# Optimization experiments

Measured on AMD Instinct MI355X. Metric: run time of the kernel, lower is better.

Reference implementation:

```python
import jax, jax.numpy as jnp
import numpy as np
from jax import lax

B, C, H, W = 4, 256, 64, 64
K = 9          # points
G = 32         # GroupNorm groups
EPS = 1e-5


def base_offset():
    # matches get_base_offset: y = 0, x in [-(K-1)//2 .. K//2], interleaved (y,x)
    bx = jnp.arange(-((K - 1) // 2), K // 2 + 1, dtype=jnp.float32)
    by = jnp.zeros_like(bx)
    return jnp.stack([by, bx], axis=1).reshape(1, 2 * K, 1, 1)


def conv3x3(x, w, b):
    y = lax.conv_general_dilated(x, w, (1, 1), ((1, 1), (1, 1)),
                                 dimension_numbers=('NCHW', 'OIHW', 'NCHW'))
    return y + b[None, :, None, None]


def group_norm(x, gamma, beta):
    b, c, h, w = x.shape
    xg = x.reshape(b, G, c // G, h, w)
    mu = xg.mean(axis=(2, 3, 4), keepdims=True)
    var = xg.var(axis=(2, 3, 4), keepdims=True)
    xn = ((xg - mu) * lax.rsqrt(var + EPS)).reshape(b, c, h, w)
    return xn * gamma[None, :, None, None] + beta[None, :, None, None]


def _deform_sample_one(img, off):
    # img: [C,H,W]; off: [K,2,H,W] (y,x). Kernel [1,K], stride 1, pad (0, K//2).
    c, h, w = img.shape
    base_x = (jnp.arange(K) - K // 2).astype(img.dtype)  # kernel grid x positions
    py = off[:, 0] + jnp.arange(h, dtype=img.dtype)[None, :, None]                 # [K,H,W]
    px = off[:, 1] + jnp.arange(w, dtype=img.dtype)[None, None, :] + base_x[:, None, None]
    y0 = jnp.floor(py)
    x0 = jnp.floor(px)
    wy = py - y0
    wx = px - x0
    flat = img.reshape(c, h * w)

    def corner(yi, xi):
        valid = (yi >= 0) & (yi <= h - 1) & (xi >= 0) & (xi <= w - 1)
        yc = jnp.clip(yi, 0, h - 1).astype(jnp.int32)
        xc = jnp.clip(xi, 0, w - 1).astype(jnp.int32)
        v = flat[:, (yc * w + xc).reshape(-1)].reshape(c, K, h, w)
        return v * valid[None].astype(img.dtype)

    return (corner(y0, x0) * ((1 - wy) * (1 - wx))[None]
            + corner(y0, x0 + 1) * ((1 - wy) * wx)[None]
            + corner(y0 + 1, x0) * (wy * (1 - wx))[None]
            + corner(y0 + 1, x0 + 1) * (wy * wx)[None])  # [C,K,H,W]


def deform_conv(x, offset, w):
    # x [B,C,H,W]; offset [B,2K,H,W]; w [O,C,1,K]; no bias (mmcv DeformConv2d)
    b, _, h, ww = x.shape
    off = offset.reshape(b, K, 2, h, ww)
    cols = jax.vmap(_deform_sample_one)(x, off)  # [B,C,K,H,W]
    return jnp.einsum('bckhw,ock->bohw', cols, w[:, :, 0, :])


def setup_inputs() -> dict:
    key = jax.random.key(0)
    ks = jax.random.split(key, 8)
    return {
        'cls_feat': jax.random.normal(ks[0], (B, C, H, W), jnp.float32),
        'reg_feat': jax.random.normal(ks[1], (B, C, H, W), jnp.float32),
        'offc_w': jax.random.normal(ks[2], (C, C, 3, 3), jnp.float32) * 0.01,
        'offc_b': jnp.zeros((C,), jnp.float32),
        'offc_g': jnp.ones((C,), jnp.float32),
        'offc_bt': jnp.zeros((C,), jnp.float32),
        'offo_w': jax.random.normal(ks[3], (2 * K, C, 3, 3), jnp.float32) * 0.01,
        'offo_b': jnp.zeros((2 * K,), jnp.float32),
        'clsdc_w': jax.random.normal(ks[4], (C, C, 1, K), jnp.float32) / np.sqrt(C * K),
        'cls_g': jnp.ones((C,), jnp.float32),
        'cls_bt': jnp.zeros((C,), jnp.float32),
        'regdc_w': jax.random.normal(ks[5], (C, C, 1, K), jnp.float32) / np.sqrt(C * K),
        'reg_g': jnp.ones((C,), jnp.float32),
        'reg_bt': jnp.zeros((C,), jnp.float32),
    }


def reference(cls_feat, reg_feat, offc_w, offc_b, offc_g, offc_bt,
              offo_w, offo_b, clsdc_w, cls_g, cls_bt, regdc_w, reg_g, reg_bt):
    # offset branch: ConvModule(3x3) -> GN -> ReLU, then 3x3 offset_out head
    t = jax.nn.relu(group_norm(conv3x3(reg_feat, offc_w, offc_b), offc_g, offc_bt))
    pts = conv3x3(t, offo_w, offo_b)          # [B, 2K, H, W]
    off = pts - base_offset()
    cls_out = jax.nn.relu(group_norm(deform_conv(cls_feat, off, clsdc_w), cls_g, cls_bt))
    reg_out = jax.nn.relu(group_norm(deform_conv(reg_feat, off, regdc_w), reg_g, reg_bt))
    return pts, cls_out, reg_out
```

## Files before the change

### kernel.cpp

```cpp
#include <hip/hip_runtime.h>
#include <math.h>

#define BB 4
#define CC 256
#define HH 64
#define WW 64
#define KP 9
#define GG 32
#define HWW (HH*WW)
#define FEL ((size_t)BB*CC*HH*WW)
#define GN_CNT 32768.0f

typedef __bf16 bf16x8 __attribute__((ext_vector_type(8)));
typedef float  f32x4  __attribute__((ext_vector_type(4)));

__device__ __forceinline__ float bflo(unsigned u) {
    union { unsigned u; float f; } x; x.u = u << 16; return x.f;
}
__device__ __forceinline__ float bfhi(unsigned u) {
    union { unsigned u; float f; } x; x.u = u & 0xffff0000u; return x.f;
}

#define VT256_RD(row, P)  (((row) << 8) + ((((P) ^ ((row) & 7))) << 3))
#define VT256_WR(row, u)  (((row) << 8) + (((((u) >> 1) ^ ((row) & 7))) << 3) + (((u) & 1) << 2))
#define VT128_RD(row, P)  (((row) << 7) + ((((P) ^ ((row) & 7))) << 3))
#define VT128_WR(row, u)  (((row) << 7) + (((((u) >> 1) ^ ((row) & 7))) << 3) + (((u) & 1) << 2))

__global__ void prep_all(const float* __restrict__ w1, const float* __restrict__ wc,
                         const float* __restrict__ wr, const float* __restrict__ w18,
                         __bf16* __restrict__ f1, __bf16* __restrict__ fc,
                         __bf16* __restrict__ fr, __bf16* __restrict__ f18,
                         float* __restrict__ stats) {
    int gid = blockIdx.x * 256 + threadIdx.x;
    if (gid < 768) stats[gid] = 0.f;
    const int NW = 589824;
    if (gid < 3 * NW) {
        int which = gid / NW;
        int idx = gid - which * NW;
        int j   = idx & 7;
        int l   = (idx >> 3) & 63;
        int o16 = (idx >> 9) & 15;
        int c0  = (idx >> 13) & 7;
        int k   = idx >> 16;
        int o = o16 * 16 + (l & 15);
        int c = c0 * 32 + (l >> 4) * 8 + j;
        const float* src = (which == 0) ? w1 : ((which == 1) ? wc : wr);
        __bf16* dst = (which == 0) ? f1 : ((which == 1) ? fc : fr);
        dst[idx] = (__bf16)src[(size_t)(o * 256 + c) * 9 + k];
    } else {
        int idx = gid - 3 * NW;
        int j   = idx & 7;
        int l   = (idx >> 3) & 63;
        int o16 = (idx >> 9) & 1;
        int c0  = (idx >> 10) & 7;
        int k   = idx >> 13;
        int o = o16 * 16 + (l & 15);
        int c = c0 * 32 + (l >> 4) * 8 + j;
        float v = (o < 18) ? w18[(size_t)(o * 256 + c) * 9 + k] : 0.f;
        f18[idx] = (__bf16)v;
    }
}

__global__ void transpose_feat(const float* __restrict__ cls,
                               const float* __restrict__ reg,
                               __bf16* __restrict__ out_cls,
                               __bf16* __restrict__ out_reg) {
    __shared__ float tile[64][65];
    int c0 = blockIdx.x * 64;
    int y  = blockIdx.y;
    int b  = blockIdx.z & 3;
    const float* in = (blockIdx.z >> 2) ? reg : cls;
    __bf16* out     = (blockIdx.z >> 2) ? out_reg : out_cls;
    int lx = threadIdx.x & 63;
    int q  = threadIdx.x >> 6;
    for (int j = 0; j < 16; ++j) {
        int ci = q * 16 + j;
        tile[ci][lx] = in[(((size_t)b*CC + c0 + ci)*HH + y)*WW + lx];
    }
    __syncthreads();
    for (int j = 0; j < 16; ++j) {
        int xi = q * 16 + j;
        out[(((size_t)b*HH + y)*WW + xi)*CC + c0 + lx] = (__bf16)tile[lx][xi];
    }
}

__global__ __launch_bounds__(256, 4) void conv1_mfma(
    const __bf16* __restrict__ in_cl,
    const __bf16* __restrict__ wf,
    const float* __restrict__ bias,
    __bf16* __restrict__ t_out,
    float* __restrict__ stats)
{
    __shared__ __bf16 Vt[66 * 256];
    __shared__ float groupStats[64];
    int blk = blockIdx.x;
    int bb = blk & 3;
    int oq = (blk >> 2) & 3;
    int y  = blk >> 4;
    int t  = threadIdx.x;
    int w  = t >> 6;
    int l  = t & 63;
    int quad = l >> 4;
    int l15  = l & 15;
    if (t < 64) groupStats[t] = 0.f;

    const __bf16* inb = in_cl + (size_t)bb * HWW * CC;
    f32x4 acc[4];
    #pragma unroll
    for (int i = 0; i < 4; ++i) acc[i] = (f32x4){0.f, 0.f, 0.f, 0.f};

    for (int ky = 0; ky < 3; ++ky) {
        int yy = y + ky - 1;
        bool yok = (yy >= 0 && yy < HH);
        __syncthreads();
        for (int u = t; u < 66 * 64; u += 256) {
            int xl = u >> 6, cu = u & 63;
            int gx = xl - 1;
            uint2 val = make_uint2(0u, 0u);
            if (yok && gx >= 0 && gx < WW)
                val = *(const uint2*)(inb + ((size_t)(yy * WW + gx)) * CC + cu * 4);
            *(uint2*)&Vt[VT256_WR(xl, cu)] = val;
        }
        __syncthreads();
        #pragma unroll
        for (int kx = 0; kx < 3; ++kx) {
            int k = ky * 3 + kx;
            const bf16x8* wbase = (const bf16x8*)(wf + (size_t)k * 65536);
            for (int c0 = 0; c0 < 8; ++c0) {
                bf16x8 a[4];
                #pragma unroll
                for (int pt = 0; pt < 4; ++pt) {
                    int row = pt * 16 + l15 + kx;
                    a[pt] = *(const bf16x8*)&Vt[VT256_RD(row, c0 * 4 + quad)];
                }
                bf16x8 bfr = wbase[(c0 * 16 + (oq * 4 + w)) * 64 + l];
                #pragma unroll
                for (int pt = 0; pt < 4; ++pt)
                    acc[pt] = __builtin_amdgcn_mfma_f32_16x16x32_bf16(
                        a[pt], bfr, acc[pt], 0, 0, 0);
            }
        }
    }
    {
        int o = oq * 64 + w * 16 + l15;
        float bi = bias[o];
        float s1 = 0.f, s2 = 0.f;
        #pragma unroll
        for (int pt = 0; pt < 4; ++pt)
            #pragma unroll
            for (int r = 0; r < 4; ++r) {
                float v = acc[pt][r] + bi;
                int px = pt * 16 + quad * 4 + r;
                t_out[(((size_t)bb * HH + y) * WW + px) * CC + o] = (__bf16)v;
                s1 += v; s2 += v * v;
            }
        s1 += __shfl_xor(s1, 16, 64); s1 += __shfl_xor(s1, 32, 64);
        s2 += __shfl_xor(s2, 16, 64); s2 += __shfl_xor(s2, 32, 64);
        if (quad == 0) {
            atomicAdd(&groupStats[(o >> 3) * 2],     s1);
            atomicAdd(&groupStats[(o >> 3) * 2 + 1], s2);
        }
    }
    __syncthreads();
    if (t < 64) atomicAdd(&stats[bb * 64 + t], groupStats[t]);
}

__global__ __launch_bounds__(256, 4) void conv18_mfma(
    const __bf16* __restrict__ t_bf,
    const __bf16* __restrict__ wf18,
    const float* __restrict__ bias,
    const float* __restrict__ stats,
    const float* __restrict__ gamma, const float* __restrict__ beta,
    float* __restrict__ pts)
{
    __shared__ __bf16 Vt[34 * 256];
    int blk = blockIdx.x;
    int bb = blk & 3;
    int xh = (blk >> 2) & 1;
    int y  = blk >> 3;
    int t  = threadIdx.x;
    int w  = t >> 6;
    int l  = t & 63;
    int quad = l >> 4;
    int l15  = l & 15;
    int mt   = w & 1;
    int o16  = w >> 1;
    int x0   = xh * 32;
    const __bf16* inb = t_bf + (size_t)bb * HWW * CC;

    int cbase = (t & 63) * 4;
    int g = cbase >> 3;
    float mu = stats[bb * 64 + g * 2]     * (1.f / GN_CNT);
    float ms = stats[bb * 64 + g * 2 + 1] * (1.f / GN_CNT);
    float rs = rsqrtf(ms - mu * mu + 1e-5f);
    float sc[4], sh[4];
    #pragma unroll
    for (int j = 0; j < 4; ++j) {
        float ga = gamma[cbase + j];
        sc[j] = rs * ga;
        sh[j] = beta[cbase + j] - mu * rs * ga;
    }

    f32x4 acc = (f32x4){0.f, 0.f, 0.f, 0.f};

    for (int ky = 0; ky < 3; ++ky) {
        int yy = y + ky - 1;
        bool yok = (yy >= 0 && yy < HH);
        __syncthreads();
        for (int u = t; u < 34 * 64; u += 256) {
            int xl = u >> 6, cu = u & 63;
            int gx = x0 - 1 + xl;
            uint2 val = make_uint2(0u, 0u);
            if (yok && gx >= 0 && gx < WW) {
                uint2 q = *(const uint2*)(inb + ((size_t)(yy * WW + gx)) * CC + cu * 4);
                float v0 = fmaxf(bflo(q.x) * sc[0] + sh[0], 0.f);
                float v1 = fmaxf(bfhi(q.x) * sc[1] + sh[1], 0.f);
                float v2 = fmaxf(bflo(q.y) * sc[2] + sh[2], 0.f);
                float v3 = fmaxf(bfhi(q.y) * sc[3] + sh[3], 0.f);
                __bf16 o4[4] = {(__bf16)v0, (__bf16)v1, (__bf16)v2, (__bf16)v3};
                val = *(const uint2*)o4;
            }
            *(uint2*)&Vt[VT256_WR(xl, cu)] = val;
        }
        __syncthreads();
        #pragma unroll
        for (int kx = 0; kx < 3; ++kx) {
            int k = ky * 3 + kx;
            const bf16x8* wbase = (const bf16x8*)(wf18 + (size_t)k * 8192);
            for (int c0 = 0; c0 < 8; ++c0) {
                int row = mt * 16 + l15 + kx;
                bf16x8 a = *(const bf16x8*)&Vt[VT256_RD(row, c0 * 4 + quad)];
                bf16x8 bfr = wbase[(c0 * 2 + o16) * 64 + l];
                acc = __builtin_amdgcn_mfma_f32_16x16x32_bf16(a, bfr, acc, 0, 0, 0);
            }
        }
    }
    {
        int o = o16 * 16 + l15;
        if (o < 18) {
            float bi = bias[o];
            float4 st;
            st.x = acc[0] + bi;
            st.y = acc[1] + bi;
            st.z = acc[2] + bi;
            st.w = acc[3] + bi;
            *(float4*)(pts + (((size_t)bb*18 + o)*HH + y)*WW + x0 + mt*16 + quad*4) = st;
        }
    }
}

__global__ __launch_bounds__(512, 4) void deform_mfma(
    const __bf16* __restrict__ cls_cl, const __bf16* __restrict__ reg_cl,
    const __bf16* __restrict__ wfc, const __bf16* __restrict__ wfr,
    const float* __restrict__ pts,
    __bf16* __restrict__ out_cls, __bf16* __restrict__ out_reg,
    float* __restrict__ stats)
{
    __shared__ float pairW4[576 * 4];
    __shared__ int   pairO4[576 * 4];
    __shared__ __bf16 Vt[2][64 * 128];
    __shared__ float groupStats[64];

    int blk = blockIdx.x;
    int g8  = blk & 7;
    int which = g8 & 1;
    int bb  = g8 >> 1;
    int y   = blk >> 3;
    const __bf16* featb = (which ? reg_cl : cls_cl) + (size_t)bb * HWW * CC;
    const __bf16* wf    = which ? wfr : wfc;
    __bf16* outp  = which ? out_reg : out_cls;
    float* statsP = stats + 256 + which * 256 + bb * 64;

    int t = threadIdx.x;
    int w = t >> 6;
    int l = t & 63;
    int quad = l >> 4;
    int l15  = l & 15;
    int tp   = t >> 5;
    int cq   = t & 31;

    if (t < 64) groupStats[t] = 0.f;
    for (int j = t; j < 576; j += 512) {
        int k = j >> 6;
        int x = j & 63;
        float py  = pts[(((size_t)bb*18 + 2*k)*HH + y)*WW + x] + (float)y;
        float pxf = pts[(((size_t)bb*18 + 2*k + 1)*HH + y)*WW + x] + (float)x;
        float y0f = floorf(py), x0f = floorf(pxf);
        float wy = py - y0f, wx = pxf - x0f;
        int iy0 = (int)y0f, ix0 = (int)x0f;
        int iy1 = iy0 + 1,  ix1 = ix0 + 1;
        bool vy0 = (iy0 >= 0 && iy0 < HH), vy1 = (iy1 >= 0 && iy1 < HH);
        bool vx0 = (ix0 >= 0 && ix0 < WW), vx1 = (ix1 >= 0 && ix1 < WW);
        int cy0 = min(max(iy0, 0), HH-1), cy1 = min(max(iy1, 0), HH-1);
        int cx0 = min(max(ix0, 0), WW-1), cx1 = min(max(ix1, 0), WW-1);
        pairW4[j*4+0] = (1.f-wy)*(1.f-wx) * ((vy0 && vx0) ? 1.f : 0.f);
        pairW4[j*4+1] = (1.f-wy)*wx       * ((vy0 && vx1) ? 1.f : 0.f);
        pairW4[j*4+2] = wy*(1.f-wx)       * ((vy1 && vx0) ? 1.f : 0.f);
        pairW4[j*4+3] = wy*wx             * ((vy1 && vx1) ? 1.f : 0.f);
        pairO4[j*4+0] = (cy0*WW + cx0)*CC;
        pairO4[j*4+1] = (cy0*WW + cx1)*CC;
        pairO4[j*4+2] = (cy1*WW + cx0)*CC;
        pairO4[j*4+3] = (cy1*WW + cx1)*CC;
    }

    f32x4 acc[2][4];
    #pragma unroll
    for (int i = 0; i < 2; ++i)
        #pragma unroll
        for (int j = 0; j < 4; ++j)
            acc[i][j] = (f32x4){0.f, 0.f, 0.f, 0.f};

    auto stage_loads = [&](int s, uint2 L[4][4], float4 WV[4]) {
        int k = s >> 1, ch = s & 1;
        const __bf16* fb = featb + ch * 128 + cq * 4;
        #pragma unroll
        for (int it = 0; it < 4; ++it) {
            int pxi = it * 16 + tp;
            int j = k * 64 + pxi;
            WV[it] = *(const float4*)&pairW4[j * 4];
            int4 ov = *(const int4*)&pairO4[j * 4];
            L[it][0] = *(const uint2*)(fb + ov.x);
            L[it][1] = *(const uint2*)(fb + ov.y);
            L[it][2] = *(const uint2*)(fb + ov.z);
            L[it][3] = *(const uint2*)(fb + ov.w);
        }
    };
    auto stage_combine = [&](int s, uint2 L[4][4], float4 WV[4]) {
        __bf16* buf = &Vt[s & 1][0];
        #pragma unroll
        for (int it = 0; it < 4; ++it) {
            int pxi = it * 16 + tp;
            float4 wv = WV[it];
            float v0 = wv.x*bflo(L[it][0].x) + wv.y*bflo(L[it][1].x) + wv.z*bflo(L[it][2].x) + wv.w*bflo(L[it][3].x);
            float v1 = wv.x*bfhi(L[it][0].x) + wv.y*bfhi(L[it][1].x) + wv.z*bfhi(L[it][2].x) + wv.w*bfhi(L[it][3].x);
            float v2 = wv.x*bflo(L[it][0].y) + wv.y*bflo(L[it][1].y) + wv.z*bflo(L[it][2].y) + wv.w*bflo(L[it][3].y);
            float v3 = wv.x*bfhi(L[it][0].y) + wv.y*bfhi(L[it][1].y) + wv.z*bfhi(L[it][2].y) + wv.w*bfhi(L[it][3].y);
            __bf16 o4[4] = {(__bf16)v0, (__bf16)v1, (__bf16)v2, (__bf16)v3};
            *(uint2*)&buf[VT128_WR(pxi, cq)] = *(const uint2*)o4;
        }
    };
    auto stage_mfma = [&](int s) {
        int k = s >> 1, ch = s & 1;
        const __bf16* buf = &Vt[s & 1][0];
        const bf16x8* wbase = (const bf16x8*)(wf + (size_t)k * 65536);
        #pragma unroll
        for (int u = 0; u < 4; ++u) {
            int c0g = ch * 4 + u;
            bf16x8 a[4], bfr[2];
            #pragma unroll
            for (int pt = 0; pt < 4; ++pt)
                a[pt] = *(const bf16x8*)&buf[VT128_RD(pt * 16 + l15, u * 4 + quad)];
            #pragma unroll
            for (int ot = 0; ot < 2; ++ot)
                bfr[ot] = wbase[(c0g * 16 + (w * 2 + ot)) * 64 + l];
            #pragma unroll
            for (int ot = 0; ot < 2; ++ot)
                #pragma unroll
                for (int pt = 0; pt < 4; ++pt)
                    acc[ot][pt] = __builtin_amdgcn_mfma_f32_16x16x32_bf16(
                        bfr[ot], a[pt], acc[ot][pt], 0, 0, 0);
        }
    };

    __syncthreads();
    {
        uint2 L[4][4]; float4 WV[4];
        stage_loads(0, L, WV);
        stage_combine(0, L, WV);
    }
    #pragma unroll 1
    for (int s = 1; s < 18; ++s) {
        __syncthreads();
        uint2 L[4][4]; float4 WV[4];
        stage_loads(s, L, WV);
        stage_mfma(s - 1);
        stage_combine(s, L, WV);
    }
    __syncthreads();
    stage_mfma(17);

    #pragma unroll
    for (int ot = 0; ot < 2; ++ot)
        #pragma unroll
        for (int r = 0; r < 4; ++r) {
            int o = w * 32 + ot * 16 + quad * 4 + r;
            __bf16* orow = outp + ((size_t)(bb*CC + o))*HWW + y*WW + l15;
            float s1 = 0.f, s2 = 0.f;
            #pragma unroll
            for (int pt = 0; pt < 4; ++pt) {
                float v = acc[ot][pt][r];
                orow[pt * 16] = (__bf16)v;
                s1 += v; s2 += v * v;
            }
            s1 += __shfl_xor(s1, 1, 64); s1 += __shfl_xor(s1, 2, 64);
            s1 += __shfl_xor(s1, 4, 64); s1 += __shfl_xor(s1, 8, 64);
            s2 += __shfl_xor(s2, 1, 64); s2 += __shfl_xor(s2, 2, 64);
            s2 += __shfl_xor(s2, 4, 64); s2 += __shfl_xor(s2, 8, 64);
            if (l15 == 0) {
                atomicAdd(&groupStats[(o >> 3) * 2],     s1);
                atomicAdd(&groupStats[(o >> 3) * 2 + 1], s2);
            }
        }
    __syncthreads();
    if (t < 64) atomicAdd(&statsP[t], groupStats[t]);
}

__global__ void gn_relu_nchw(const __bf16* __restrict__ in_cls, const __bf16* __restrict__ in_reg,
                             float* __restrict__ out_cls, float* __restrict__ out_reg,
                             const float* __restrict__ stats_base,
                             const float* __restrict__ gcls, const float* __restrict__ bcls,
                             const float* __restrict__ greg, const float* __restrict__ breg) {
    int which = blockIdx.y;
    const __bf16* in = which ? in_reg  : in_cls;
    float* out       = which ? out_reg : out_cls;
    const float* st  = stats_base + (which ? 512 : 256);
    const float* gg  = which ? greg : gcls;
    const float* be  = which ? breg : bcls;
    size_t e = ((size_t)blockIdx.x * 256 + threadIdx.x) * 8;
    int c = (int)((e >> 12) & 255);
    int b = (int)(e >> 20);
    int g = c >> 3;
    float mu = st[(b*32 + g)*2] * (1.f / GN_CNT);
    float ms = st[(b*32 + g)*2 + 1] * (1.f / GN_CNT);
    float rs = rsqrtf(ms - mu*mu + 1e-5f);
    float ga = gg[c], bb = be[c];
    uint4 q = *(const uint4*)(in + e);
    float v[8] = {bflo(q.x), bfhi(q.x), bflo(q.y), bfhi(q.y),
                  bflo(q.z), bfhi(q.z), bflo(q.w), bfhi(q.w)};
    float4 r0, r1;
    r0.x = fmaxf((v[0] - mu)*rs*ga + bb, 0.f);
    r0.y = fmaxf((v[1] - mu)*rs*ga + bb, 0.f);
    r0.z = fmaxf((v[2] - mu)*rs*ga + bb, 0.f);
    r0.w = fmaxf((v[3] - mu)*rs*ga + bb, 0.f);
    r1.x = fmaxf((v[4] - mu)*rs*ga + bb, 0.f);
    r1.y = fmaxf((v[5] - mu)*rs*ga + bb, 0.f);
    r1.z = fmaxf((v[6] - mu)*rs*ga + bb, 0.f);
    r1.w = fmaxf((v[7] - mu)*rs*ga + bb, 0.f);
    *(float4*)(out + e)     = r0;
    *(float4*)(out + e + 4) = r1;
}

extern "C" void kernel_launch(void* const* d_in, const int* in_sizes, int n_in,
                              void* d_out, int out_size, void* d_ws, size_t ws_size,
                              hipStream_t stream) {
    (void)in_sizes; (void)n_in; (void)out_size; (void)ws_size;
    const float* cls_feat = (const float*)d_in[0];
    const float* reg_feat = (const float*)d_in[1];
    const float* offc_w   = (const float*)d_in[2];
    const float* offc_b   = (const float*)d_in[3];
    const float* offc_g   = (const float*)d_in[4];
    const float* offc_bt  = (const float*)d_in[5];
    const float* offo_w   = (const float*)d_in[6];
    const float* offo_b   = (const float*)d_in[7];
    const float* clsdc_w  = (const float*)d_in[8];
    const float* cls_g    = (const float*)d_in[9];
    const float* cls_bt   = (const float*)d_in[10];
    const float* regdc_w  = (const float*)d_in[11];
    const float* reg_g    = (const float*)d_in[12];
    const float* reg_bt   = (const float*)d_in[13];
    float* out = (float*)d_out;

    char* ws = (char*)d_ws;
    __bf16* reg_cl = (__bf16*)ws;
    __bf16* cls_cl = (__bf16*)(ws + 8388608);
    __bf16* t_bf   = (__bf16*)(ws + 16777216);
    __bf16* dc_cls = (__bf16*)(ws + 25165824);
    __bf16* dc_reg = (__bf16*)(ws + 33554432);
    __bf16* wt1f   = (__bf16*)(ws + 41943040);
    __bf16* wtcf   = (__bf16*)(ws + 41943040 + 1179648);
    __bf16* wtrf   = (__bf16*)(ws + 41943040 + 2359296);
    __bf16* wf18   = (__bf16*)(ws + 41943040 + 3538944);
    float*  stats  = (float*)(ws + 41943040 + 3686400);

    float* pts     = out;
    float* out_cls = out + 294912;
    float* out_reg = out + 294912 + FEL;

    hipLaunchKernelGGL(prep_all, dim3(7200), dim3(256), 0, stream,
                       offc_w, clsdc_w, regdc_w, offo_w, wt1f, wtcf, wtrf, wf18, stats);
    hipLaunchKernelGGL(transpose_feat, dim3(4, 64, 8), dim3(256), 0, stream,
                       cls_feat, reg_feat, cls_cl, reg_cl);
    hipLaunchKernelGGL(conv1_mfma, dim3(1024), dim3(256), 0, stream,
                       reg_cl, wt1f, offc_b, t_bf, stats);
    hipLaunchKernelGGL(conv18_mfma, dim3(512), dim3(256), 0, stream,
                       t_bf, wf18, offo_b, stats, offc_g, offc_bt, pts);
    hipLaunchKernelGGL(deform_mfma, dim3(512), dim3(512), 0, stream,
                       cls_cl, reg_cl, wtcf, wtrf, pts, dc_cls, dc_reg, stats);
    hipLaunchKernelGGL(gn_relu_nchw, dim3(2048, 2), dim3(256), 0, stream,
                       dc_cls, dc_reg, out_cls, out_reg,
                       stats, cls_g, cls_bt, reg_g, reg_bt);
}
```

Measured before the change: 255.3 us.

## Widen deform gathers to 16B, preload weights to registers, fence scheduling

```diff
diff --git a/kernel.cpp b/kernel.cpp
--- a/kernel.cpp
+++ b/kernel.cpp
@@ -24,7 +24,6 @@
 #define VT256_RD(row, P)  (((row) << 8) + ((((P) ^ ((row) & 7))) << 3))
 #define VT256_WR(row, u)  (((row) << 8) + (((((u) >> 1) ^ ((row) & 7))) << 3) + (((u) & 1) << 2))
 #define VT128_RD(row, P)  (((row) << 7) + ((((P) ^ ((row) & 7))) << 3))
-#define VT128_WR(row, u)  (((row) << 7) + (((((u) >> 1) ^ ((row) & 7))) << 3) + (((u) & 1) << 2))
 
 __global__ void prep_all(const float* __restrict__ w1, const float* __restrict__ wc,
                          const float* __restrict__ wr, const float* __restrict__ w18,
@@ -276,8 +275,8 @@
     int l = t & 63;
     int quad = l >> 4;
     int l15  = l & 15;
-    int tp   = t >> 5;
-    int cq   = t & 31;
+    int cq4  = t & 15;
+    int pxg  = t >> 4;
 
     if (t < 64) groupStats[t] = 0.f;
     for (int j = t; j < 576; j += 512) {
@@ -310,73 +309,86 @@
         for (int j = 0; j < 4; ++j)
             acc[i][j] = (f32x4){0.f, 0.f, 0.f, 0.f};
 
-    auto stage_loads = [&](int s, uint2 L[4][4], float4 WV[4]) {
+    bf16x8 wreg[4][2];
+    uint4  L[2][4];
+
+    auto gathers = [&](int s) {
         int k = s >> 1, ch = s & 1;
-        const __bf16* fb = featb + ch * 128 + cq * 4;
-        #pragma unroll
-        for (int it = 0; it < 4; ++it) {
-            int pxi = it * 16 + tp;
-            int j = k * 64 + pxi;
-            WV[it] = *(const float4*)&pairW4[j * 4];
+        const __bf16* fb = featb + ch * 128 + cq4 * 8;
+        #pragma unroll
+        for (int it = 0; it < 2; ++it) {
+            int j = k * 64 + it * 32 + pxg;
             int4 ov = *(const int4*)&pairO4[j * 4];
-            L[it][0] = *(const uint2*)(fb + ov.x);
-            L[it][1] = *(const uint2*)(fb + ov.y);
-            L[it][2] = *(const uint2*)(fb + ov.z);
-            L[it][3] = *(const uint2*)(fb + ov.w);
+            L[it][0] = *(const uint4*)(fb + ov.x);
+            L[it][1] = *(const uint4*)(fb + ov.y);
+            L[it][2] = *(const uint4*)(fb + ov.z);
+            L[it][3] = *(const uint4*)(fb + ov.w);
         }
     };
-    auto stage_combine = [&](int s, uint2 L[4][4], float4 WV[4]) {
-        __bf16* buf = &Vt[s & 1][0];
-        #pragma unroll
-        for (int it = 0; it < 4; ++it) {
-            int pxi = it * 16 + tp;
-            float4 wv = WV[it];
-            float v0 = wv.x*bflo(L[it][0].x) + wv.y*bflo(L[it][1].x) + wv.z*bflo(L[it][2].x) + wv.w*bflo(L[it][3].x);
-            float v1 = wv.x*bfhi(L[it][0].x) + wv.y*bfhi(L[it][1].x) + wv.z*bfhi(L[it][2].x) + wv.w*bfhi(L[it][3].x);
-            float v2 = wv.x*bflo(L[it][0].y) + wv.y*bflo(L[it][1].y) + wv.z*bflo(L[it][2].y) + wv.w*bflo(L[it][3].y);
-            float v3 = wv.x*bfhi(L[it][0].y) + wv.y*bfhi(L[it][1].y) + wv.z*bfhi(L[it][2].y) + wv.w*bfhi(L[it][3].y);
-            __bf16 o4[4] = {(__bf16)v0, (__bf16)v1, (__bf16)v2, (__bf16)v3};
-            *(uint2*)&buf[VT128_WR(pxi, cq)] = *(const uint2*)o4;
-        }
+    auto wloads = [&](int s) {
+        int k = s >> 1, ch = s & 1;
+        const bf16x8* wbase = (const bf16x8*)(wf + (size_t)k * 65536);
+        #pragma unroll
+        for (int u = 0; u < 4; ++u)
+            #pragma unroll
+            for (int ot = 0; ot < 2; ++ot)
+                wreg[u][ot] = wbase[(((ch * 4 + u) * 16) + (w * 2 + ot)) * 64 + l];
     };
     auto stage_mfma = [&](int s) {
-        int k = s >> 1, ch = s & 1;
         const __bf16* buf = &Vt[s & 1][0];
-        const bf16x8* wbase = (const bf16x8*)(wf + (size_t)k * 65536);
         #pragma unroll
         for (int u = 0; u < 4; ++u) {
-            int c0g = ch * 4 + u;
-            bf16x8 a[4], bfr[2];
+            bf16x8 a[4];
             #pragma unroll
             for (int pt = 0; pt < 4; ++pt)
                 a[pt] = *(const bf16x8*)&buf[VT128_RD(pt * 16 + l15, u * 4 + quad)];
             #pragma unroll
             for (int ot = 0; ot < 2; ++ot)
-                bfr[ot] = wbase[(c0g * 16 + (w * 2 + ot)) * 64 + l];
-            #pragma unroll
-            for (int ot = 0; ot < 2; ++ot)
                 #pragma unroll
                 for (int pt = 0; pt < 4; ++pt)
                     acc[ot][pt] = __builtin_amdgcn_mfma_f32_16x16x32_bf16(
-                        bfr[ot], a[pt], acc[ot][pt], 0, 0, 0);
+                        wreg[u][ot], a[pt], acc[ot][pt], 0, 0, 0);
         }
     };
+    auto combine = [&](int s) {
+        __bf16* buf = &Vt[s & 1][0];
+        int k = s >> 1;
+        #pragma unroll
+        for (int it = 0; it < 2; ++it) {
+            int pxi = it * 32 + pxg;
+            int j = k * 64 + pxi;
+            float4 wv = *(const float4*)&pairW4[j * 4];
+            __bf16 o8[8];
+            #pragma unroll
+            for (int h = 0; h < 4; ++h) {
+                unsigned q0 = ((const unsigned*)&L[it][0])[h];
+                unsigned q1 = ((const unsigned*)&L[it][1])[h];
+                unsigned q2 = ((const unsigned*)&L[it][2])[h];
+                unsigned q3 = ((const unsigned*)&L[it][3])[h];
+                float lo = wv.x*bflo(q0) + wv.y*bflo(q1) + wv.z*bflo(q2) + wv.w*bflo(q3);
+                float hi = wv.x*bfhi(q0) + wv.y*bfhi(q1) + wv.z*bfhi(q2) + wv.w*bfhi(q3);
+                o8[h*2]   = (__bf16)lo;
+                o8[h*2+1] = (__bf16)hi;
+            }
+            *(uint4*)&buf[VT128_RD(pxi, cq4)] = *(const uint4*)o8;
+        }
+    };
 
     __syncthreads();
-    {
-        uint2 L[4][4]; float4 WV[4];
-        stage_loads(0, L, WV);
-        stage_combine(0, L, WV);
-    }
+    gathers(0);
+    combine(0);
     #pragma unroll 1
     for (int s = 1; s < 18; ++s) {
         __syncthreads();
-        uint2 L[4][4]; float4 WV[4];
-        stage_loads(s, L, WV);
+        wloads(s - 1);
+        gathers(s);
+        __builtin_amdgcn_sched_barrier(0);
         stage_mfma(s - 1);
-        stage_combine(s, L, WV);
+        __builtin_amdgcn_sched_barrier(0);
+        combine(s);
     }
     __syncthreads();
+    wloads(17);
     stage_mfma(17);
 
     #pragma unroll
```

Measured after the change: 419.4 us. 1.64x slower.
